# Kernel tuning notes

Measured on AMD Instinct MI355X. Metric: run time of the kernel, lower is better.

The kernel has to match this reference:

```python
import jax, jax.numpy as jnp
import numpy as np

B, S, D, H = 2, 2048, 1024, 16


def setup_inputs() -> dict:
    key = jax.random.key(0)
    kq, kk, kv, kw = jax.random.split(key, 4)
    Q = jax.random.normal(kq, (B, S, D), dtype=jnp.float32)
    K = jax.random.normal(kk, (B, S, D), dtype=jnp.float32)
    V = jax.random.normal(kv, (B, S, D), dtype=jnp.float32)
    Wo = jax.random.normal(kw, (D, D), dtype=jnp.float32) * (1.0 / np.sqrt(D))
    return {"Q": Q, "K": K, "V": V, "Wo": Wo, "num_heads": H}


def reference(Q, K, V, Wo, num_heads):
    b, s, d = Q.shape
    dk = d // num_heads
    # split heads: [B,S,D] -> [B,H,S,dk]
    q = Q.reshape(b, s, num_heads, dk).transpose(0, 2, 1, 3)
    k = K.reshape(b, s, num_heads, dk).transpose(0, 2, 1, 3)
    v = V.reshape(b, s, num_heads, dk).transpose(0, 2, 1, 3)
    scale = 1.0 / jnp.sqrt(jnp.asarray(dk, dtype=q.dtype))
    logits = jnp.einsum('bhqd,bhkd->bhqk', q, k) * scale  # [B,H,S,S]
    probs = jax.nn.softmax(logits, axis=-1).astype(q.dtype)
    o = jnp.einsum('bhqk,bhkd->bhqd', probs, v)  # [B,H,S,dk]
    o = o.transpose(0, 2, 1, 3).reshape(b, s, d)  # concat heads
    # O = einsum('d dkh, ... dkh -> ... d', Wo, scores) == scores @ Wo^T
    return jnp.einsum('dk,bsk->bsd', Wo, o)
```

## Files before the change

### kernel.cpp

```cpp
#include <hip/hip_runtime.h>
#include <hip/hip_bf16.h>

#define B_ 2
#define S_ 2048
#define D_ 1024
#define H_ 16
#define DK_ 64

typedef __hip_bfloat16 bf16;
typedef short v8s __attribute__((ext_vector_type(8)));
typedef short v4s __attribute__((ext_vector_type(4)));
typedef float v4f __attribute__((ext_vector_type(4)));
typedef float v16f __attribute__((ext_vector_type(16)));
typedef int   v4i __attribute__((ext_vector_type(4)));
typedef int   v2i __attribute__((ext_vector_type(2)));

static __device__ __forceinline__ v16f mfma32(v8s a, v8s b, v16f c) {
  return __builtin_amdgcn_mfma_f32_32x32x16_bf16(a, b, c, 0, 0, 0);
}
static __device__ __forceinline__ void gl2lds16(const void* g, void* l) {
  __builtin_amdgcn_global_load_lds((const __attribute__((address_space(1))) void*)g,
                                   (__attribute__((address_space(3))) void*)l,
                                   16, 0, 0);
}
static __device__ __forceinline__ short f2bf(float x) {
  return (short)__builtin_bit_cast(unsigned short, __float2bfloat16(x));
}
static __device__ __forceinline__ int pk2f(float lo, float hi) {
  unsigned a = __builtin_bit_cast(unsigned, lo) + 0x8000u;
  unsigned b = __builtin_bit_cast(unsigned, hi) + 0x8000u;
  return (int)__builtin_amdgcn_perm(b, a, 0x07060302u);
}
static __device__ __forceinline__ float bf2f(short s) {
  return __builtin_bit_cast(float, ((unsigned)(unsigned short)s) << 16);
}

__global__ __launch_bounds__(256) void pre_kernel(
    const float* __restrict__ K, const float* __restrict__ V,
    const float* __restrict__ Wo, bf16* __restrict__ Kb,
    bf16* __restrict__ Vt, bf16* __restrict__ Wb)
{
  __shared__ __align__(16) bf16 td[64 * 72];
  const int t = threadIdx.x;
  const int bx = blockIdx.x;

  if (bx < 2048) {
    const int idx = bx * 256 + t;
    const int seg = idx & 7;
    const int rest = idx >> 3;
    const int h = rest & 15;
    const int bs = rest >> 4;
    const float* src = K + (size_t)bs * D_ + h * 64 + seg * 8;
    v4f x = *(const v4f*)src, y = *(const v4f*)(src + 4);
    v8s r;
    r[0]=f2bf(x[0]); r[1]=f2bf(x[1]); r[2]=f2bf(x[2]); r[3]=f2bf(x[3]);
    r[4]=f2bf(y[0]); r[5]=f2bf(y[1]); r[6]=f2bf(y[2]); r[7]=f2bf(y[3]);
    const int b = bs >> 11, s = bs & 2047;
    *(v8s*)(Kb + ((size_t)(b * H_ + h) * S_ + s) * DK_ + seg * 8) = r;
  } else if (bx < 3072) {
    const int idx = bx - 2048;
    const int bh = idx >> 5, b = bh >> 4, h = bh & 15;
    const int s0 = (idx & 31) * 64;
    const int srow = t >> 2;
    const int cs = t & 3;
    const float* vp = V + (size_t)(b * S_ + s0 + srow) * D_ + h * 64 + cs * 16;
#pragma unroll
    for (int j = 0; j < 4; j++) {
      v4f x = *(const v4f*)(vp + j * 4);
#pragma unroll
      for (int jj = 0; jj < 4; jj++)
        td[(cs * 16 + j * 4 + jj) * 72 + srow] = __float2bfloat16(x[jj]);
    }
    __syncthreads();
    const int d = t >> 2;
#pragma unroll
    for (int a2 = 0; a2 < 4; a2++) {
      const int pos = cs * 16 + a2 * 4;
      const int g = pos >> 5;
      const int a = (pos >> 2) & 7;
      const int kbase = g * 32 + ((a >> 2) << 4) + ((a & 1) << 3) + (((a >> 1) & 1) << 2);
      v4s val = *(const v4s*)(td + d * 72 + kbase);
      *(v4s*)(Vt + ((size_t)bh * DK_ + d) * S_ + s0 + pos) = val;
    }
  } else {
    const int i = ((bx - 3072) * 256 + t) * 4;
    v4f a = *(const v4f*)(Wo + i);
    v4s r;
    r[0]=f2bf(a[0]); r[1]=f2bf(a[1]); r[2]=f2bf(a[2]); r[3]=f2bf(a[3]);
    *(v4s*)((short*)Wb + i) = r;
  }
}

__global__ __launch_bounds__(256, 4) void attn4_kernel(
    const float* __restrict__ Q, const bf16* __restrict__ Kb,
    const bf16* __restrict__ Vt, bf16* __restrict__ Op0,
    bf16* __restrict__ Op1, float* __restrict__ Lp)
{
  __shared__ __align__(16) bf16 kk[2][64 * 64];
  __shared__ __align__(16) bf16 vv[2][64 * 64];

  const int t = threadIdx.x;
  const int w = t >> 6, l = t & 63, h2 = l >> 5, ln = l & 31;
  const int bh = blockIdx.x, b = bh >> 4, h = bh & 15;
  const int qbase = blockIdx.y * 128 + w * 32;
  const int z = blockIdx.z;
  const int kb0 = z << 10;

  const bf16* Kbh = Kb + (size_t)bh * (S_ * DK_);
  const bf16* Vbh = Vt + (size_t)bh * (DK_ * S_);

  const float sc = 0.18033688011112042f;
  v8s bq[4];
  {
    const float* qp = Q + ((size_t)b * S_ + qbase + ln) * D_ + h * DK_ + h2 * 8;
#pragma unroll
    for (int c = 0; c < 4; c++) {
      v4f x = *(const v4f*)(qp + c * 16);
      v4f y = *(const v4f*)(qp + c * 16 + 4);
      v4i r = { pk2f(x[0]*sc, x[1]*sc), pk2f(x[2]*sc, x[3]*sc),
                pk2f(y[0]*sc, y[1]*sc), pk2f(y[2]*sc, y[3]*sc) };
      bq[c] = __builtin_bit_cast(v8s, r);
    }
  }

  v16f accA, accB;
#pragma unroll
  for (int r = 0; r < 16; r++) { accA[r] = 0.f; accB[r] = 0.f; }
  float lpart = 0.f;

#pragma unroll
  for (int j = 0; j < 2; j++) {
    const int flat = j * 256 + t, row = flat >> 3, sp = flat & 7;
    gl2lds16(Kbh + (size_t)(kb0 + row) * DK_ + ((sp ^ (row & 7)) * 8), &kk[0][flat * 8]);
    gl2lds16(Vbh + (size_t)row * S_ + kb0 + ((sp ^ (row & 7)) * 8), &vv[0][flat * 8]);
  }

  int it = 0;
  for (int kb = kb0; kb < kb0 + 1024; kb += 64, it ^= 1) {
    __syncthreads();
    if (kb + 64 < kb0 + 1024) {
#pragma unroll
      for (int j = 0; j < 2; j++) {
        const int flat = j * 256 + t, row = flat >> 3, sp = flat & 7;
        gl2lds16(Kbh + (size_t)(kb + 64 + row) * DK_ + ((sp ^ (row & 7)) * 8),
                 &kk[it ^ 1][flat * 8]);
        gl2lds16(Vbh + (size_t)row * S_ + (kb + 64) + ((sp ^ (row & 7)) * 8),
                 &vv[it ^ 1][flat * 8]);
      }
    }
    const bf16* kc_ = kk[it];
    const bf16* vc_ = vv[it];

    v16f s0, s1;
#pragma unroll
    for (int r = 0; r < 16; r++) { s0[r] = 0.f; s1[r] = 0.f; }
#pragma unroll
    for (int c = 0; c < 4; c++) {
      const int sd = 2 * c + h2;
      v8s a0 = *(const v8s*)(kc_ + ln * 64 + ((sd ^ (ln & 7)) * 8));
      v8s a1 = *(const v8s*)(kc_ + (32 + ln) * 64 + ((sd ^ (ln & 7)) * 8));
      s0 = mfma32(a0, bq[c], s0);
      s1 = mfma32(a1, bq[c], s1);
    }

    float p0[16], p1[16];
#pragma unroll
    for (int r = 0; r < 16; r++) { p0[r] = exp2f(s0[r]); p1[r] = exp2f(s1[r]); }
    float su = 0.f;
#pragma unroll
    for (int r = 0; r < 16; r++) su += p0[r] + p1[r];
    lpart += su;

    v4i i00 = { pk2f(p0[0],p0[1]),  pk2f(p0[2],p0[3]),  pk2f(p0[4],p0[5]),  pk2f(p0[6],p0[7]) };
    v4i i01 = { pk2f(p0[8],p0[9]),  pk2f(p0[10],p0[11]),pk2f(p0[12],p0[13]),pk2f(p0[14],p0[15]) };
    v4i i10 = { pk2f(p1[0],p1[1]),  pk2f(p1[2],p1[3]),  pk2f(p1[4],p1[5]),  pk2f(p1[6],p1[7]) };
    v4i i11 = { pk2f(p1[8],p1[9]),  pk2f(p1[10],p1[11]),pk2f(p1[12],p1[13]),pk2f(p1[14],p1[15]) };
    v8s pb00 = __builtin_bit_cast(v8s, i00);
    v8s pb01 = __builtin_bit_cast(v8s, i01);
    v8s pb10 = __builtin_bit_cast(v8s, i10);
    v8s pb11 = __builtin_bit_cast(v8s, i11);

#pragma unroll
    for (int st = 0; st < 2; st++) {
#pragma unroll
      for (int kc = 0; kc < 2; kc++) {
        const int q = st * 4 + kc * 2 + h2;
        v8s avA = *(const v8s*)(vc_ + ln * 64 + ((q ^ (ln & 7)) * 8));
        v8s avB = *(const v8s*)(vc_ + (32 + ln) * 64 + ((q ^ (ln & 7)) * 8));
        v8s pb = st ? (kc ? pb11 : pb10) : (kc ? pb01 : pb00);
        accA = mfma32(avA, pb, accA);
        accB = mfma32(avB, pb, accB);
      }
    }
  }

  __syncthreads();
  const float lfull = lpart + __shfl_xor(lpart, 32);
  const float linv = 1.0f / lfull;
  bf16* epw = &kk[0][0] + w * 2048;
#pragma unroll
  for (int r = 0; r < 16; r += 4) {
    const int off = 4 * h2;
    const int sgA = (r >> 2) ^ (ln & 3);
    const int sgB = 4 + sgA;
    v2i pa = { pk2f(accA[r]*linv,   accA[r+1]*linv),
               pk2f(accA[r+2]*linv, accA[r+3]*linv) };
    v2i pb = { pk2f(accB[r]*linv,   accB[r+1]*linv),
               pk2f(accB[r+2]*linv, accB[r+3]*linv) };
    *(v2i*)(epw + ln * 64 + sgA * 8 + off) = pa;
    *(v2i*)(epw + ln * 64 + sgB * 8 + off) = pb;
  }
  if (h2 == 0)
    Lp[((size_t)z * 32 + bh) * S_ + qbase + ln] = lfull;

  bf16* Op = z ? Op1 : Op0;
#pragma unroll
  for (int i = 0; i < 4; i++) {
    const int flat = i * 64 + l;
    const int qr = flat >> 3, sd = flat & 7;
    const int phys = ((sd & 3) ^ (qr & 3)) | (sd & 4);
    v8s val = *(const v8s*)(epw - w * 2048 + (w * 32 + qr) * 64 + phys * 8);
    *(v8s*)(Op + ((size_t)b * S_ + qbase - w * 32 + w * 32 + qr) * D_ + h * DK_ + sd * 8) = val;
  }
}

__global__ __launch_bounds__(256) void merge_kernel(
    const bf16* __restrict__ Op0, const bf16* __restrict__ Op1,
    const float* __restrict__ Lp, bf16* __restrict__ O)
{
  const int flat = blockIdx.x * 256 + threadIdx.x;
  const int qrow = flat >> 7;
  const int seg = flat & 127;
  const int b = qrow >> 11, s = qrow & 2047;
  const int h = seg >> 3;
  const int bh = b * H_ + h;
  const float l0 = Lp[(size_t)bh * S_ + s];
  const float l1 = Lp[(size_t)(32 + bh) * S_ + s];
  const float inv = 1.0f / (l0 + l1);
  const float w0 = l0 * inv, w1 = l1 * inv;
  const size_t off = (size_t)qrow * D_ + seg * 8;
  v8s a = *(const v8s*)(Op0 + off);
  v8s c = *(const v8s*)(Op1 + off);
  v4i r;
#pragma unroll
  for (int j = 0; j < 4; j++) {
    float lo = w0 * bf2f(a[2*j])   + w1 * bf2f(c[2*j]);
    float hi = w0 * bf2f(a[2*j+1]) + w1 * bf2f(c[2*j+1]);
    r[j] = pk2f(lo, hi);
  }
  *(v8s*)(O + off) = __builtin_bit_cast(v8s, r);
}

__global__ __launch_bounds__(256, 4) void proj3_kernel(
    const bf16* __restrict__ A, const bf16* __restrict__ Wo, float* __restrict__ Out)
{
  __shared__ __align__(16) bf16 aa[2][64 * 64];
  __shared__ __align__(16) bf16 bb[2][64 * 64];

  const int t = threadIdx.x;
  const int w = t >> 6, l = t & 63, h2 = l >> 5, ln = l & 31;
  const int m0 = blockIdx.x * 64, n0 = blockIdx.y * 64;
  const int wm = (w & 1) * 32, wn = (w >> 1) * 32;

  v16f acc;
#pragma unroll
  for (int r = 0; r < 16; r++) acc[r] = 0.f;

#pragma unroll
  for (int j = 0; j < 2; j++) {
    const int flat = j * 256 + t, row = flat >> 3, sp = flat & 7;
    gl2lds16(A  + (size_t)(m0 + row) * D_ + ((sp ^ (row & 7)) * 8), &aa[0][flat * 8]);
    gl2lds16(Wo + (size_t)(n0 + row) * D_ + ((sp ^ (row & 7)) * 8), &bb[0][flat * 8]);
  }

  int it = 0;
  for (int k0 = 0; k0 < D_; k0 += 64, it ^= 1) {
    __syncthreads();
    if (k0 + 64 < D_) {
#pragma unroll
      for (int j = 0; j < 2; j++) {
        const int flat = j * 256 + t, row = flat >> 3, sp = flat & 7;
        gl2lds16(A  + (size_t)(m0 + row) * D_ + (k0 + 64) + ((sp ^ (row & 7)) * 8),
                 &aa[it ^ 1][flat * 8]);
        gl2lds16(Wo + (size_t)(n0 + row) * D_ + (k0 + 64) + ((sp ^ (row & 7)) * 8),
                 &bb[it ^ 1][flat * 8]);
      }
    }
    const bf16* ac = aa[it];
    const bf16* bc = bb[it];
#pragma unroll
    for (int c = 0; c < 4; c++) {
      const int sd = 2 * c + h2;
      v8s av = *(const v8s*)(ac + (wm + ln) * 64 + ((sd ^ (ln & 7)) * 8));
      v8s bv = *(const v8s*)(bc + (wn + ln) * 64 + ((sd ^ (ln & 7)) * 8));
      acc = mfma32(av, bv, acc);
    }
  }

#pragma unroll
  for (int r = 0; r < 16; r++) {
    const int row = m0 + wm + (r & 3) + 4 * h2 + 8 * (r >> 2);
    Out[(size_t)row * D_ + n0 + wn + ln] = acc[r];
  }
}

extern "C" void kernel_launch(void* const* d_in, const int* in_sizes, int n_in,
                              void* d_out, int out_size, void* d_ws, size_t ws_size,
                              hipStream_t stream) {
  (void)in_sizes; (void)n_in; (void)out_size; (void)ws_size;
  const float* Q  = (const float*)d_in[0];
  const float* K  = (const float*)d_in[1];
  const float* V  = (const float*)d_in[2];
  const float* Wo = (const float*)d_in[3];
  float* out = (float*)d_out;

  bf16* base = (bf16*)d_ws;
  bf16* kb   = base;
  bf16* vt   = base + (size_t)4  * 1024 * 1024;
  bf16* wo_b = base + (size_t)8  * 1024 * 1024;
  bf16* op0  = base + (size_t)9  * 1024 * 1024;
  bf16* op1  = base + (size_t)13 * 1024 * 1024;
  float* lp  = (float*)(base + (size_t)17 * 1024 * 1024);
  bf16* ows  = kb;

  pre_kernel  <<<dim3(4096),       256, 0, stream>>>(K, V, Wo, kb, vt, wo_b);
  attn4_kernel<<<dim3(32, 16, 2),  256, 0, stream>>>(Q, kb, vt, op0, op1, lp);
  merge_kernel<<<dim3(2048),       256, 0, stream>>>(op0, op1, lp, ows);
  proj3_kernel<<<dim3(64, 16),     256, 0, stream>>>(ows, wo_b, out);
}
```

Baseline: 176.8 us.

## Remap attention blocks per XCD, add MFMA priority, retile projection to 128x128

The attention grid is flattened to 1D and remapped so each XCD handles the blocks of a few (batch, head) pairs, which keeps their K/V in that XCD's L2. MFMA sections get raised wave priority, and the first QK MFMA accumulates from a constant zero instead of re-zeroing per tile. Normalisation by the partial row sum is dropped in attention and the merge divides once by the combined sum, which is mathematically the same. The output projection moves to 128x128 tiles with 512 threads and two accumulators per wave for more operand reuse, at the cost of fewer blocks (256) and one block per CU.

```diff
diff --git a/kernel.cpp b/kernel.cpp
--- a/kernel.cpp
+++ b/kernel.cpp
@@ -101,9 +101,16 @@
 
   const int t = threadIdx.x;
   const int w = t >> 6, l = t & 63, h2 = l >> 5, ln = l & 31;
-  const int bh = blockIdx.x, b = bh >> 4, h = bh & 15;
-  const int qbase = blockIdx.y * 128 + w * 32;
-  const int z = blockIdx.z;
+
+  const int bid = blockIdx.x;
+  const int xcd = bid & 7;
+  const int idx = bid >> 3;
+  const int bh  = xcd * 4 + (idx >> 5);
+  const int rest = idx & 31;
+  const int qt = rest & 15, z = rest >> 4;
+
+  const int b = bh >> 4, h = bh & 15;
+  const int qbase = qt * 128 + w * 32;
   const int kb0 = z << 10;
 
   const bf16* Kbh = Kb + (size_t)bh * (S_ * DK_);
@@ -122,6 +129,10 @@
       bq[c] = __builtin_bit_cast(v8s, r);
     }
   }
+
+  v16f Z;
+#pragma unroll
+  for (int r = 0; r < 16; r++) Z[r] = 0.f;
 
   v16f accA, accB;
 #pragma unroll
@@ -152,24 +163,29 @@
     const bf16* vc_ = vv[it];
 
     v16f s0, s1;
-#pragma unroll
-    for (int r = 0; r < 16; r++) { s0[r] = 0.f; s1[r] = 0.f; }
+    __builtin_amdgcn_s_setprio(1);
 #pragma unroll
     for (int c = 0; c < 4; c++) {
       const int sd = 2 * c + h2;
       v8s a0 = *(const v8s*)(kc_ + ln * 64 + ((sd ^ (ln & 7)) * 8));
       v8s a1 = *(const v8s*)(kc_ + (32 + ln) * 64 + ((sd ^ (ln & 7)) * 8));
-      s0 = mfma32(a0, bq[c], s0);
-      s1 = mfma32(a1, bq[c], s1);
-    }
+      if (c == 0) {
+        s0 = mfma32(a0, bq[0], Z);
+        s1 = mfma32(a1, bq[0], Z);
+      } else {
+        s0 = mfma32(a0, bq[c], s0);
+        s1 = mfma32(a1, bq[c], s1);
+      }
+    }
+    __builtin_amdgcn_s_setprio(0);
 
     float p0[16], p1[16];
 #pragma unroll
     for (int r = 0; r < 16; r++) { p0[r] = exp2f(s0[r]); p1[r] = exp2f(s1[r]); }
-    float su = 0.f;
-#pragma unroll
-    for (int r = 0; r < 16; r++) su += p0[r] + p1[r];
-    lpart += su;
+    float suA = 0.f, suB = 0.f;
+#pragma unroll
+    for (int r = 0; r < 16; r++) { suA += p0[r]; suB += p1[r]; }
+    lpart += suA + suB;
 
     v4i i00 = { pk2f(p0[0],p0[1]),  pk2f(p0[2],p0[3]),  pk2f(p0[4],p0[5]),  pk2f(p0[6],p0[7]) };
     v4i i01 = { pk2f(p0[8],p0[9]),  pk2f(p0[10],p0[11]),pk2f(p0[12],p0[13]),pk2f(p0[14],p0[15]) };
@@ -180,6 +196,7 @@
     v8s pb10 = __builtin_bit_cast(v8s, i10);
     v8s pb11 = __builtin_bit_cast(v8s, i11);
 
+    __builtin_amdgcn_s_setprio(1);
 #pragma unroll
     for (int st = 0; st < 2; st++) {
 #pragma unroll
@@ -192,21 +209,21 @@
         accB = mfma32(avB, pb, accB);
       }
     }
+    __builtin_amdgcn_s_setprio(0);
   }
 
   __syncthreads();
   const float lfull = lpart + __shfl_xor(lpart, 32);
-  const float linv = 1.0f / lfull;
   bf16* epw = &kk[0][0] + w * 2048;
 #pragma unroll
   for (int r = 0; r < 16; r += 4) {
     const int off = 4 * h2;
     const int sgA = (r >> 2) ^ (ln & 3);
     const int sgB = 4 + sgA;
-    v2i pa = { pk2f(accA[r]*linv,   accA[r+1]*linv),
-               pk2f(accA[r+2]*linv, accA[r+3]*linv) };
-    v2i pb = { pk2f(accB[r]*linv,   accB[r+1]*linv),
-               pk2f(accB[r+2]*linv, accB[r+3]*linv) };
+    v2i pa = { pk2f(accA[r],   accA[r+1]),
+               pk2f(accA[r+2], accA[r+3]) };
+    v2i pb = { pk2f(accB[r],   accB[r+1]),
+               pk2f(accB[r+2], accB[r+3]) };
     *(v2i*)(epw + ln * 64 + sgA * 8 + off) = pa;
     *(v2i*)(epw + ln * 64 + sgB * 8 + off) = pb;
   }
@@ -237,70 +254,72 @@
   const float l0 = Lp[(size_t)bh * S_ + s];
   const float l1 = Lp[(size_t)(32 + bh) * S_ + s];
   const float inv = 1.0f / (l0 + l1);
-  const float w0 = l0 * inv, w1 = l1 * inv;
   const size_t off = (size_t)qrow * D_ + seg * 8;
   v8s a = *(const v8s*)(Op0 + off);
   v8s c = *(const v8s*)(Op1 + off);
   v4i r;
 #pragma unroll
   for (int j = 0; j < 4; j++) {
-    float lo = w0 * bf2f(a[2*j])   + w1 * bf2f(c[2*j]);
-    float hi = w0 * bf2f(a[2*j+1]) + w1 * bf2f(c[2*j+1]);
+    float lo = (bf2f(a[2*j])   + bf2f(c[2*j]))   * inv;
+    float hi = (bf2f(a[2*j+1]) + bf2f(c[2*j+1])) * inv;
     r[j] = pk2f(lo, hi);
   }
   *(v8s*)(O + off) = __builtin_bit_cast(v8s, r);
 }
 
-__global__ __launch_bounds__(256, 4) void proj3_kernel(
+__global__ __launch_bounds__(512, 1) void projm_kernel(
     const bf16* __restrict__ A, const bf16* __restrict__ Wo, float* __restrict__ Out)
 {
-  __shared__ __align__(16) bf16 aa[2][64 * 64];
-  __shared__ __align__(16) bf16 bb[2][64 * 64];
+  __shared__ __align__(16) bf16 aa[2][128 * 64];
+  __shared__ __align__(16) bf16 bb[2][128 * 64];
 
   const int t = threadIdx.x;
   const int w = t >> 6, l = t & 63, h2 = l >> 5, ln = l & 31;
-  const int m0 = blockIdx.x * 64, n0 = blockIdx.y * 64;
-  const int wm = (w & 1) * 32, wn = (w >> 1) * 32;
-
-  v16f acc;
-#pragma unroll
-  for (int r = 0; r < 16; r++) acc[r] = 0.f;
-
-#pragma unroll
-  for (int j = 0; j < 2; j++) {
-    const int flat = j * 256 + t, row = flat >> 3, sp = flat & 7;
-    gl2lds16(A  + (size_t)(m0 + row) * D_ + ((sp ^ (row & 7)) * 8), &aa[0][flat * 8]);
-    gl2lds16(Wo + (size_t)(n0 + row) * D_ + ((sp ^ (row & 7)) * 8), &bb[0][flat * 8]);
-  }
+  const int m0 = blockIdx.x * 128, n0 = blockIdx.y * 128;
+  const int wm = (w & 3) * 32;
+  const int wn = (w >> 2) * 64;
+
+  v16f acc0, acc1;
+#pragma unroll
+  for (int r = 0; r < 16; r++) { acc0[r] = 0.f; acc1[r] = 0.f; }
+
+  auto stage = [&](int k0, int buf) {
+#pragma unroll
+    for (int j = 0; j < 2; j++) {
+      const int flat = j * 512 + t, row = flat >> 3, sp = flat & 7;
+      gl2lds16(A  + (size_t)(m0 + row) * D_ + k0 + ((sp ^ (row & 7)) * 8),
+               &aa[buf][flat * 8]);
+      gl2lds16(Wo + (size_t)(n0 + row) * D_ + k0 + ((sp ^ (row & 7)) * 8),
+               &bb[buf][flat * 8]);
+    }
+  };
+
+  stage(0, 0);
 
   int it = 0;
   for (int k0 = 0; k0 < D_; k0 += 64, it ^= 1) {
     __syncthreads();
-    if (k0 + 64 < D_) {
-#pragma unroll
-      for (int j = 0; j < 2; j++) {
-        const int flat = j * 256 + t, row = flat >> 3, sp = flat & 7;
-        gl2lds16(A  + (size_t)(m0 + row) * D_ + (k0 + 64) + ((sp ^ (row & 7)) * 8),
-                 &aa[it ^ 1][flat * 8]);
-        gl2lds16(Wo + (size_t)(n0 + row) * D_ + (k0 + 64) + ((sp ^ (row & 7)) * 8),
-                 &bb[it ^ 1][flat * 8]);
-      }
-    }
+    if (k0 + 64 < D_) stage(k0 + 64, it ^ 1);
     const bf16* ac = aa[it];
     const bf16* bc = bb[it];
 #pragma unroll
     for (int c = 0; c < 4; c++) {
       const int sd = 2 * c + h2;
-      v8s av = *(const v8s*)(ac + (wm + ln) * 64 + ((sd ^ (ln & 7)) * 8));
-      v8s bv = *(const v8s*)(bc + (wn + ln) * 64 + ((sd ^ (ln & 7)) * 8));
-      acc = mfma32(av, bv, acc);
+      const int x0 = (sd ^ (ln & 7)) * 8;
+      v8s a  = *(const v8s*)(ac + (wm + ln) * 64 + x0);
+      v8s b0 = *(const v8s*)(bc + (wn + ln) * 64 + x0);
+      v8s b1 = *(const v8s*)(bc + (wn + 32 + ln) * 64 + x0);
+      acc0 = mfma32(a, b0, acc0);
+      acc1 = mfma32(a, b1, acc1);
     }
   }
 
 #pragma unroll
   for (int r = 0; r < 16; r++) {
-    const int row = m0 + wm + (r & 3) + 4 * h2 + 8 * (r >> 2);
-    Out[(size_t)row * D_ + n0 + wn + ln] = acc[r];
+    const int rr = (r & 3) + 4 * h2 + 8 * (r >> 2);
+    float* o = Out + (size_t)(m0 + wm + rr) * D_ + n0 + wn;
+    o[ln]      = acc0[r];
+    o[32 + ln] = acc1[r];
   }
 }
 
@@ -324,7 +343,7 @@
   bf16* ows  = kb;
 
   pre_kernel  <<<dim3(4096),       256, 0, stream>>>(K, V, Wo, kb, vt, wo_b);
-  attn4_kernel<<<dim3(32, 16, 2),  256, 0, stream>>>(Q, kb, vt, op0, op1, lp);
+  attn4_kernel<<<dim3(1024),       256, 0, stream>>>(Q, kb, vt, op0, op1, lp);
   merge_kernel<<<dim3(2048),       256, 0, stream>>>(op0, op1, lp, ows);
-  proj3_kernel<<<dim3(64, 16),     256, 0, stream>>>(ows, wo_b, out);
-}
+  projm_kernel<<<dim3(32, 8),      512, 0, stream>>>(ows, wo_b, out);
+}
```

New measurement: 176.7 us. About the same (-0.1%).
